# Optimization experiments

Hardware: AMD Instinct MI355X
Metric: run time of the kernel (lower is better)

The kernel has to match this reference:

```python
import jax, jax.numpy as jnp
import numpy as np

GRAY = 0.2989 + 0.5870 + 0.1140  # tf.image.rgb_to_grayscale weight sum (channels identical after grayscale_to_rgb)


def _resample(img, coords, axis):
    """Bilinear 1-D resample of `img` along `axis` at float `coords` (clamped)."""
    n = img.shape[axis]
    i0f = jnp.floor(coords)
    i0 = jnp.clip(i0f, 0, n - 1).astype(jnp.int32)
    i1 = jnp.clip(i0f + 1.0, 0, n - 1).astype(jnp.int32)
    f = coords - i0f
    a = jnp.take(img, i0, axis=axis)
    b = jnp.take(img, i1, axis=axis)
    shp = [1] * img.ndim
    shp[axis] = -1
    f = f.reshape(shp)
    return a * (1.0 - f) + b * f


def _aug_one(img, off_f, b, c, size, docrop, flp, k):
    S = img.shape[0]
    # ---- random crop (prob 0.5) + bilinear resize back to SxS (half-pixel centers) ----
    size_f = jnp.where(docrop, size.astype(jnp.float32), float(S))
    off = jnp.where(docrop, jnp.floor(off_f * (S - size_f + 1.0)), 0.0)  # [2] integer-valued offsets
    idx = (jnp.arange(S, dtype=jnp.float32) + 0.5) * (size_f / S) - 0.5
    img = _resample(img, idx + off[0], 0)
    img = _resample(img, idx + off[1], 1)
    # ---- random flip_left_right + rot90(k) ----
    img = jnp.where(flp, img[:, ::-1, :], img)
    rots = jnp.stack([img,
                      jnp.rot90(img, 1, (0, 1)),
                      jnp.rot90(img, 2, (0, 1)),
                      jnp.rot90(img, 3, (0, 1))])
    img = rots[k]
    # ---- per-channel brightness + contrast (gray->rgb->gray round trip == GRAY scale) ----
    x = img + b  # [S,S,C] + [C]
    m = jnp.mean(x, axis=(0, 1), keepdims=True)
    x = (x - m) * c + m
    return x * GRAY


def setup_inputs() -> dict:
    B, S, C = 64, 256, 5
    key = jax.random.key(0)
    ks = jax.random.split(key, 8)
    crops = jax.random.normal(ks[0], (B, S, S, C), dtype=jnp.float32)
    crop_size = jax.random.randint(ks[1], (B,), int(0.8 * S), S, dtype=jnp.int32)
    do_crop = jax.random.uniform(ks[2], (B,)) < 0.5
    off_frac = jax.random.uniform(ks[3], (B, 2), dtype=jnp.float32)
    flip = jax.random.uniform(ks[4], (B,)) < 0.5
    rot_k = jax.random.randint(ks[5], (B,), 0, 4, dtype=jnp.int32)
    bright = jax.random.uniform(ks[6], (B, C), minval=-0.1, maxval=0.1, dtype=jnp.float32)
    contrast = jax.random.uniform(ks[7], (B, C), minval=0.8, maxval=1.2, dtype=jnp.float32)
    return {"crops": crops, "off_frac": off_frac, "bright": bright, "contrast": contrast,
            "crop_size": crop_size, "do_crop": do_crop, "flip": flip, "rot_k": rot_k}


def reference(crops, off_frac, bright, contrast, crop_size, do_crop, flip, rot_k):
    return jax.vmap(_aug_one)(crops, off_frac, bright, contrast, crop_size, do_crop, flip, rot_k)
```

## Files before the change

kernel.cpp:

```cpp
#include <hip/hip_runtime.h>
#include <math.h>

#define SDIM 256
#define CH 5
#define ROWF (SDIM * CH)
#define GRAYF 0.9999f

__global__ __launch_bounds__(256) void aug_fused_kernel(
    const float* __restrict__ crops,
    const float* __restrict__ off_frac,
    const int*   __restrict__ crop_size,
    const int*   __restrict__ do_crop,
    const int*   __restrict__ flip,
    const int*   __restrict__ rot_k,
    const float* __restrict__ bright,
    const float* __restrict__ contrast,
    float* __restrict__ out)
{
    const int tid = threadIdx.x;
    const int b   = blockIdx.x & 63;
    const int pp  = blockIdx.x >> 6;

    __shared__ __align__(16) float smem[28 * 260];
    __shared__ __align__(16) float wyl[SDIM];
    __shared__ __align__(16) float wxl[SDIM];
    __shared__ float psum[4][CH];
    __shared__ float prm[2 * CH];

    const bool  docrop = do_crop[b] != 0;
    const float size_f = docrop ? (float)crop_size[b] : 256.0f;
    const float scale  = size_f * (1.0f / 256.0f);
    const float span   = 256.0f - size_f + 1.0f;
    const float off0   = docrop ? floorf(off_frac[2 * b + 0] * span) : 0.0f;
    const float off1   = docrop ? floorf(off_frac[2 * b + 1] * span) : 0.0f;
    const int   k      = rot_k[b] & 3;
    const bool  flp    = flip[b] != 0;

    wyl[tid] = 0.0f;
    wxl[tid] = 0.0f;
    __syncthreads();
    {
        const float cy = ((float)tid + 0.5f) * scale - 0.5f + off0;
        const float fl = floorf(cy);
        const float fy = cy - fl;
        const int r0 = min(max((int)fl, 0), 255);
        const int r1 = min(max((int)fl + 1, 0), 255);
        atomicAdd(&wyl[r0], 1.0f - fy);
        atomicAdd(&wyl[r1], fy);

        const float cx = ((float)tid + 0.5f) * scale - 0.5f + off1;
        const float fl2 = floorf(cx);
        const float fx  = cx - fl2;
        const int c0 = min(max((int)fl2, 0), 255);
        const int c1 = min(max((int)fl2 + 1, 0), 255);
        atomicAdd(&wxl[c0], 1.0f - fx);
        atomicAdd(&wxl[c1], fx);
    }
    __syncthreads();

    const float* srcbase = crops + (size_t)b * SDIM * ROWF;
    float acc[5] = {0.0f, 0.0f, 0.0f, 0.0f, 0.0f};
    #pragma unroll 4
    for (int it = 0; it < 64; ++it) {
        const int m = it * 256 + tid;
        const int r = m >> 6;
        const int t = m & 63;
        const float4* p4 = reinterpret_cast<const float4*>(srcbase + r * ROWF + t * 20);
        const float4 q0 = p4[0], q1 = p4[1], q2 = p4[2], q3 = p4[3], q4 = p4[4];
        const float wr = wyl[r];
        const float4 wx = reinterpret_cast<const float4*>(wxl)[t];
        const float w0 = wx.x * wr, w1 = wx.y * wr, w2 = wx.z * wr, w3 = wx.w * wr;
        acc[0] += q0.x * w0; acc[1] += q0.y * w0; acc[2] += q0.z * w0; acc[3] += q0.w * w0;
        acc[4] += q1.x * w0; acc[0] += q1.y * w1; acc[1] += q1.z * w1; acc[2] += q1.w * w1;
        acc[3] += q2.x * w1; acc[4] += q2.y * w1; acc[0] += q2.z * w2; acc[1] += q2.w * w2;
        acc[2] += q3.x * w2; acc[3] += q3.y * w2; acc[4] += q3.z * w2; acc[0] += q3.w * w3;
        acc[1] += q4.x * w3; acc[2] += q4.y * w3; acc[3] += q4.z * w3; acc[4] += q4.w * w3;
    }

    const int lane = tid & 63;
    const int wv   = tid >> 6;
    #pragma unroll
    for (int ch = 0; ch < CH; ++ch) {
        float s = acc[ch];
        #pragma unroll
        for (int o = 32; o > 0; o >>= 1) s += __shfl_down(s, o, 64);
        if (lane == 0) psum[wv][ch] = s;
    }
    __syncthreads();
    if (tid < CH) {
        const float s  = psum[0][tid] + psum[1][tid] + psum[2][tid] + psum[3][tid];
        const float m  = s * (1.0f / 65536.0f);
        const float co = contrast[b * CH + tid];
        const float br = bright[b * CH + tid];
        prm[tid]      = co * GRAYF;
        prm[CH + tid] = ((1.0f - co) * m + br) * GRAYF;
    }

    const int rr = tid >> 6;

    for (int og = 0; og < 8; ++og) {
        const int oi0 = pp * 32 + og * 4;
        __syncthreads();

        float vout[20];

        if ((k & 1) == 0) {
            const int y_min = (k == 0) ? oi0 : 255 - (oi0 + 3);
            const float cymin = ((float)y_min + 0.5f) * scale - 0.5f + off0;
            const int rbase = (int)floorf(cymin);
            const int nst   = docrop ? 5 : 4;

            const float4* src4 = reinterpret_cast<const float4*>(srcbase);
            float4* dst4 = reinterpret_cast<float4*>(smem);
            for (int i = tid; i < nst * 320; i += 256) {
                const int w  = i / 320;
                const int f4 = i - w * 320;
                const int rc = min(max(rbase + w, 0), 255);
                dst4[i] = src4[rc * 320 + f4];
            }
            __syncthreads();

            const int oi = oi0 + rr;
            const int y  = (k == 0) ? oi : 255 - oi;

            if (!docrop) {
                const float* rb = smem + (y - rbase) * ROWF;
                #pragma unroll
                for (int p = 0; p < 4; ++p) {
                    const int oj = lane + 64 * p;
                    const int xf = (k == 0) ? oj : 255 - oj;
                    const int x  = flp ? 255 - xf : xf;
                    #pragma unroll
                    for (int ch = 0; ch < CH; ++ch) vout[p * 5 + ch] = rb[x * CH + ch];
                }
            } else {
                const float cy  = ((float)y + 0.5f) * scale - 0.5f + off0;
                const float flr = floorf(cy);
                const float fy  = cy - flr;
                const float* rbA = smem + ((int)flr - rbase) * ROWF;
                const float* rbB = rbA + ROWF;
                #pragma unroll
                for (int p = 0; p < 4; ++p) {
                    const int oj = lane + 64 * p;
                    const int xf = (k == 0) ? oj : 255 - oj;
                    const int x  = flp ? 255 - xf : xf;
                    const float cx  = ((float)x + 0.5f) * scale - 0.5f + off1;
                    const float fl2 = floorf(cx);
                    const float fx  = cx - fl2;
                    const int c0 = min(max((int)fl2, 0), 255);
                    const int c1 = min(max((int)fl2 + 1, 0), 255);
                    #pragma unroll
                    for (int ch = 0; ch < CH; ++ch) {
                        const float aV = rbA[c0 * CH + ch] + fx * (rbA[c1 * CH + ch] - rbA[c0 * CH + ch]);
                        const float dV = rbB[c0 * CH + ch] + fx * (rbB[c1 * CH + ch] - rbB[c0 * CH + ch]);
                        vout[p * 5 + ch] = aV + fy * (dV - aV);
                    }
                }
            }
        } else {
            const int xfA = (k == 1) ? 255 - oi0 : oi0;
            const int xfB = (k == 1) ? 255 - (oi0 + 3) : oi0 + 3;
            const int xA = flp ? 255 - xfA : xfA;
            const int xB = flp ? 255 - xfB : xfB;
            const int xmin = min(xA, xB);

            if (!docrop) {
                const int base4 = min((xmin * CH) & ~3, ROWF - 24);
                const float4* rp = reinterpret_cast<const float4*>(
                    srcbase + (size_t)tid * ROWF + base4);
                const float4 q0 = rp[0], q1 = rp[1], q2 = rp[2];
                const float4 q3 = rp[3], q4 = rp[4], q5 = rp[5];
                smem[ 0*260+tid]=q0.x; smem[ 1*260+tid]=q0.y; smem[ 2*260+tid]=q0.z; smem[ 3*260+tid]=q0.w;
                smem[ 4*260+tid]=q1.x; smem[ 5*260+tid]=q1.y; smem[ 6*260+tid]=q1.z; smem[ 7*260+tid]=q1.w;
                smem[ 8*260+tid]=q2.x; smem[ 9*260+tid]=q2.y; smem[10*260+tid]=q2.z; smem[11*260+tid]=q2.w;
                smem[12*260+tid]=q3.x; smem[13*260+tid]=q3.y; smem[14*260+tid]=q3.z; smem[15*260+tid]=q3.w;
                smem[16*260+tid]=q4.x; smem[17*260+tid]=q4.y; smem[18*260+tid]=q4.z; smem[19*260+tid]=q4.w;
                smem[20*260+tid]=q5.x; smem[21*260+tid]=q5.y; smem[22*260+tid]=q5.z; smem[23*260+tid]=q5.w;
                __syncthreads();

                const int oi = oi0 + rr;
                const int xf = (k == 1) ? 255 - oi : oi;
                const int x  = flp ? 255 - xf : xf;
                const int slotA = x * CH - base4;
                #pragma unroll
                for (int p = 0; p < 4; ++p) {
                    const int oj = lane + 64 * p;
                    const int y  = (k == 1) ? oj : 255 - oj;
                    #pragma unroll
                    for (int ch = 0; ch < CH; ++ch)
                        vout[p * 5 + ch] = smem[(slotA + ch) * 260 + y];
                }
            } else {
                const float cxmin = ((float)xmin + 0.5f) * scale - 0.5f + off1;
                const int cbase = (int)floorf(cxmin);
                const int base4 = (cbase * CH) & ~3;
                const bool fastp = (cbase >= 0) && (cbase + 4 <= 255) && (base4 >= 0) && (base4 + 28 <= ROWF);

                if (fastp) {
                    const float4* rp = reinterpret_cast<const float4*>(
                        srcbase + (size_t)tid * ROWF + base4);
                    const float4 q0 = rp[0], q1 = rp[1], q2 = rp[2], q3 = rp[3];
                    const float4 q4 = rp[4], q5 = rp[5], q6 = rp[6];
                    smem[ 0*260+tid]=q0.x; smem[ 1*260+tid]=q0.y; smem[ 2*260+tid]=q0.z; smem[ 3*260+tid]=q0.w;
                    smem[ 4*260+tid]=q1.x; smem[ 5*260+tid]=q1.y; smem[ 6*260+tid]=q1.z; smem[ 7*260+tid]=q1.w;
                    smem[ 8*260+tid]=q2.x; smem[ 9*260+tid]=q2.y; smem[10*260+tid]=q2.z; smem[11*260+tid]=q2.w;
                    smem[12*260+tid]=q3.x; smem[13*260+tid]=q3.y; smem[14*260+tid]=q3.z; smem[15*260+tid]=q3.w;
                    smem[16*260+tid]=q4.x; smem[17*260+tid]=q4.y; smem[18*260+tid]=q4.z; smem[19*260+tid]=q4.w;
                    smem[20*260+tid]=q5.x; smem[21*260+tid]=q5.y; smem[22*260+tid]=q5.z; smem[23*260+tid]=q5.w;
                    smem[24*260+tid]=q6.x; smem[25*260+tid]=q6.y; smem[26*260+tid]=q6.z; smem[27*260+tid]=q6.w;
                } else {
                    #pragma unroll
                    for (int w = 0; w < 28; ++w) {
                        const int f2 = base4 + w + ROWF;
                        const int c2 = f2 / 5;
                        const int ch = f2 - c2 * 5;
                        const int cc = min(max(c2 - 256, 0), 255);
                        smem[w * 260 + tid] = srcbase[(size_t)tid * ROWF + cc * CH + ch];
                    }
                }
                __syncthreads();

                const int oi = oi0 + rr;
                const int xf = (k == 1) ? 255 - oi : oi;
                const int x  = flp ? 255 - xf : xf;
                const float cx  = ((float)x + 0.5f) * scale - 0.5f + off1;
                const float fl2 = floorf(cx);
                const float fx  = cx - fl2;
                const int slotA = (int)fl2 * CH - base4;
                const int slotB = slotA + CH;

                #pragma unroll
                for (int p = 0; p < 4; ++p) {
                    const int oj = lane + 64 * p;
                    const int y  = (k == 1) ? oj : 255 - oj;
                    const float cy  = ((float)y + 0.5f) * scale - 0.5f + off0;
                    const float flr = floorf(cy);
                    const float fy  = cy - flr;
                    const int r0 = min(max((int)flr, 0), 255);
                    const int r1 = min(max((int)flr + 1, 0), 255);
                    #pragma unroll
                    for (int ch = 0; ch < CH; ++ch) {
                        const float p00 = smem[(slotA + ch) * 260 + r0];
                        const float p01 = smem[(slotB + ch) * 260 + r0];
                        const float p10 = smem[(slotA + ch) * 260 + r1];
                        const float p11 = smem[(slotB + ch) * 260 + r1];
                        const float aV = p00 + fx * (p01 - p00);
                        const float dV = p10 + fx * (p11 - p10);
                        vout[p * 5 + ch] = aV + fy * (dV - aV);
                    }
                }
            }
        }

        float aa[5], ab[5];
        #pragma unroll
        for (int ch = 0; ch < CH; ++ch) { aa[ch] = prm[ch]; ab[ch] = prm[CH + ch]; }
        #pragma unroll
        for (int p = 0; p < 4; ++p)
            #pragma unroll
            for (int ch = 0; ch < CH; ++ch)
                vout[p * 5 + ch] = vout[p * 5 + ch] * aa[ch] + ab[ch];

        __syncthreads();
        #pragma unroll
        for (int p = 0; p < 4; ++p) {
            const int oj = lane + 64 * p;
            #pragma unroll
            for (int ch = 0; ch < CH; ++ch)
                smem[rr * ROWF + oj * CH + ch] = vout[p * 5 + ch];
        }
        __syncthreads();

        const float4* ob4 = reinterpret_cast<const float4*>(smem);
        float4* dst = reinterpret_cast<float4*>(out + ((size_t)b * SDIM + oi0) * ROWF);
        #pragma unroll
        for (int q = 0; q < 5; ++q) dst[q * 256 + tid] = ob4[q * 256 + tid];
    }
}

extern "C" void kernel_launch(void* const* d_in, const int* in_sizes, int n_in,
                              void* d_out, int out_size, void* d_ws, size_t ws_size,
                              hipStream_t stream) {
    const float* crops     = (const float*)d_in[0];
    const float* off_frac  = (const float*)d_in[1];
    const float* bright    = (const float*)d_in[2];
    const float* contrast  = (const float*)d_in[3];
    const int*   crop_size = (const int*)d_in[4];
    const int*   do_crop   = (const int*)d_in[5];
    const int*   flipb     = (const int*)d_in[6];
    const int*   rot_k     = (const int*)d_in[7];

    float* out = (float*)d_out;

    aug_fused_kernel<<<dim3(512), dim3(256), 0, stream>>>(
        crops, off_frac, crop_size, do_crop, flipb, rot_k, bright, contrast, out);
}
```

Before: 228.1 us.

## Split into resample kernel with partial sums plus separate affine pass

```diff
diff --git a/kernel.cpp b/kernel.cpp
--- a/kernel.cpp
+++ b/kernel.cpp
@@ -6,26 +6,25 @@
 #define ROWF (SDIM * CH)
 #define GRAYF 0.9999f
 
-__global__ __launch_bounds__(256) void aug_fused_kernel(
+__global__ __launch_bounds__(256) void aug_out_kernel(
     const float* __restrict__ crops,
     const float* __restrict__ off_frac,
     const int*   __restrict__ crop_size,
     const int*   __restrict__ do_crop,
     const int*   __restrict__ flip,
     const int*   __restrict__ rot_k,
-    const float* __restrict__ bright,
-    const float* __restrict__ contrast,
+    float* __restrict__ part,
     float* __restrict__ out)
 {
-    const int tid = threadIdx.x;
-    const int b   = blockIdx.x & 63;
-    const int pp  = blockIdx.x >> 6;
+    const int gid  = blockIdx.x;
+    const int oi0  = gid * 4;
+    const int b    = blockIdx.y;
+    const int tid  = threadIdx.x;
+    const int rr   = tid >> 6;
+    const int lane = tid & 63;
 
     __shared__ __align__(16) float smem[28 * 260];
-    __shared__ __align__(16) float wyl[SDIM];
-    __shared__ __align__(16) float wxl[SDIM];
     __shared__ float psum[4][CH];
-    __shared__ float prm[2 * CH];
 
     const bool  docrop = do_crop[b] != 0;
     const float size_f = docrop ? (float)crop_size[b] : 256.0f;
@@ -36,246 +35,233 @@
     const int   k      = rot_k[b] & 3;
     const bool  flp    = flip[b] != 0;
 
-    wyl[tid] = 0.0f;
-    wxl[tid] = 0.0f;
-    __syncthreads();
-    {
-        const float cy = ((float)tid + 0.5f) * scale - 0.5f + off0;
-        const float fl = floorf(cy);
-        const float fy = cy - fl;
-        const int r0 = min(max((int)fl, 0), 255);
-        const int r1 = min(max((int)fl + 1, 0), 255);
-        atomicAdd(&wyl[r0], 1.0f - fy);
-        atomicAdd(&wyl[r1], fy);
-
-        const float cx = ((float)tid + 0.5f) * scale - 0.5f + off1;
-        const float fl2 = floorf(cx);
-        const float fx  = cx - fl2;
-        const int c0 = min(max((int)fl2, 0), 255);
-        const int c1 = min(max((int)fl2 + 1, 0), 255);
-        atomicAdd(&wxl[c0], 1.0f - fx);
-        atomicAdd(&wxl[c1], fx);
-    }
-    __syncthreads();
-
-    const float* srcbase = crops + (size_t)b * SDIM * ROWF;
-    float acc[5] = {0.0f, 0.0f, 0.0f, 0.0f, 0.0f};
-    #pragma unroll 4
-    for (int it = 0; it < 64; ++it) {
-        const int m = it * 256 + tid;
-        const int r = m >> 6;
-        const int t = m & 63;
-        const float4* p4 = reinterpret_cast<const float4*>(srcbase + r * ROWF + t * 20);
-        const float4 q0 = p4[0], q1 = p4[1], q2 = p4[2], q3 = p4[3], q4 = p4[4];
-        const float wr = wyl[r];
-        const float4 wx = reinterpret_cast<const float4*>(wxl)[t];
-        const float w0 = wx.x * wr, w1 = wx.y * wr, w2 = wx.z * wr, w3 = wx.w * wr;
-        acc[0] += q0.x * w0; acc[1] += q0.y * w0; acc[2] += q0.z * w0; acc[3] += q0.w * w0;
-        acc[4] += q1.x * w0; acc[0] += q1.y * w1; acc[1] += q1.z * w1; acc[2] += q1.w * w1;
-        acc[3] += q2.x * w1; acc[4] += q2.y * w1; acc[0] += q2.z * w2; acc[1] += q2.w * w2;
-        acc[2] += q3.x * w2; acc[3] += q3.y * w2; acc[4] += q3.z * w2; acc[0] += q3.w * w3;
-        acc[1] += q4.x * w3; acc[2] += q4.y * w3; acc[3] += q4.z * w3; acc[4] += q4.w * w3;
-    }
-
-    const int lane = tid & 63;
-    const int wv   = tid >> 6;
-    #pragma unroll
-    for (int ch = 0; ch < CH; ++ch) {
-        float s = acc[ch];
-        #pragma unroll
-        for (int o = 32; o > 0; o >>= 1) s += __shfl_down(s, o, 64);
-        if (lane == 0) psum[wv][ch] = s;
-    }
-    __syncthreads();
-    if (tid < CH) {
-        const float s  = psum[0][tid] + psum[1][tid] + psum[2][tid] + psum[3][tid];
-        const float m  = s * (1.0f / 65536.0f);
-        const float co = contrast[b * CH + tid];
-        const float br = bright[b * CH + tid];
-        prm[tid]      = co * GRAYF;
-        prm[CH + tid] = ((1.0f - co) * m + br) * GRAYF;
-    }
-
-    const int rr = tid >> 6;
-
-    for (int og = 0; og < 8; ++og) {
-        const int oi0 = pp * 32 + og * 4;
+    float vout[20];
+
+    if ((k & 1) == 0) {
+        const int y_min = (k == 0) ? oi0 : 255 - (oi0 + 3);
+        const float cymin = ((float)y_min + 0.5f) * scale - 0.5f + off0;
+        const int rbase = (int)floorf(cymin);
+        const int nst   = docrop ? 5 : 4;
+
+        const float4* src4 = reinterpret_cast<const float4*>(crops + (size_t)b * SDIM * ROWF);
+        float4* dst4 = reinterpret_cast<float4*>(smem);
+        for (int i = tid; i < nst * 320; i += 256) {
+            const int w  = i / 320;
+            const int f4 = i - w * 320;
+            const int rc = min(max(rbase + w, 0), 255);
+            dst4[i] = src4[rc * 320 + f4];
+        }
         __syncthreads();
 
-        float vout[20];
-
-        if ((k & 1) == 0) {
-            const int y_min = (k == 0) ? oi0 : 255 - (oi0 + 3);
-            const float cymin = ((float)y_min + 0.5f) * scale - 0.5f + off0;
-            const int rbase = (int)floorf(cymin);
-            const int nst   = docrop ? 5 : 4;
-
-            const float4* src4 = reinterpret_cast<const float4*>(srcbase);
-            float4* dst4 = reinterpret_cast<float4*>(smem);
-            for (int i = tid; i < nst * 320; i += 256) {
-                const int w  = i / 320;
-                const int f4 = i - w * 320;
-                const int rc = min(max(rbase + w, 0), 255);
-                dst4[i] = src4[rc * 320 + f4];
-            }
+        const int oi = oi0 + rr;
+        const int y  = (k == 0) ? oi : 255 - oi;
+
+        if (!docrop) {
+            const float* rb = smem + (y - rbase) * ROWF;
+            #pragma unroll
+            for (int p = 0; p < 4; ++p) {
+                const int oj = lane + 64 * p;
+                const int xf = (k == 0) ? oj : 255 - oj;
+                const int x  = flp ? 255 - xf : xf;
+                #pragma unroll
+                for (int ch = 0; ch < CH; ++ch) vout[p * 5 + ch] = rb[x * CH + ch];
+            }
+        } else {
+            const float cy  = ((float)y + 0.5f) * scale - 0.5f + off0;
+            const float flr = floorf(cy);
+            const float fy  = cy - flr;
+            const float* rbA = smem + ((int)flr - rbase) * ROWF;
+            const float* rbB = rbA + ROWF;
+            #pragma unroll
+            for (int p = 0; p < 4; ++p) {
+                const int oj = lane + 64 * p;
+                const int xf = (k == 0) ? oj : 255 - oj;
+                const int x  = flp ? 255 - xf : xf;
+                const float cx  = ((float)x + 0.5f) * scale - 0.5f + off1;
+                const float fl2 = floorf(cx);
+                const float fx  = cx - fl2;
+                const int c0 = min(max((int)fl2, 0), 255);
+                const int c1 = min(max((int)fl2 + 1, 0), 255);
+                #pragma unroll
+                for (int ch = 0; ch < CH; ++ch) {
+                    const float aV = rbA[c0 * CH + ch] + fx * (rbA[c1 * CH + ch] - rbA[c0 * CH + ch]);
+                    const float dV = rbB[c0 * CH + ch] + fx * (rbB[c1 * CH + ch] - rbB[c0 * CH + ch]);
+                    vout[p * 5 + ch] = aV + fy * (dV - aV);
+                }
+            }
+        }
+    } else {
+        const int xfA = (k == 1) ? 255 - oi0 : oi0;
+        const int xfB = (k == 1) ? 255 - (oi0 + 3) : oi0 + 3;
+        const int xA = flp ? 255 - xfA : xfA;
+        const int xB = flp ? 255 - xfB : xfB;
+        const int xmin = min(xA, xB);
+
+        if (!docrop) {
+            const int base4 = min((xmin * CH) & ~3, ROWF - 24);
+            const float4* rp = reinterpret_cast<const float4*>(
+                crops + ((size_t)b * SDIM + tid) * ROWF + base4);
+            const float4 q0 = rp[0], q1 = rp[1], q2 = rp[2];
+            const float4 q3 = rp[3], q4 = rp[4], q5 = rp[5];
+            smem[ 0*260+tid]=q0.x; smem[ 1*260+tid]=q0.y; smem[ 2*260+tid]=q0.z; smem[ 3*260+tid]=q0.w;
+            smem[ 4*260+tid]=q1.x; smem[ 5*260+tid]=q1.y; smem[ 6*260+tid]=q1.z; smem[ 7*260+tid]=q1.w;
+            smem[ 8*260+tid]=q2.x; smem[ 9*260+tid]=q2.y; smem[10*260+tid]=q2.z; smem[11*260+tid]=q2.w;
+            smem[12*260+tid]=q3.x; smem[13*260+tid]=q3.y; smem[14*260+tid]=q3.z; smem[15*260+tid]=q3.w;
+            smem[16*260+tid]=q4.x; smem[17*260+tid]=q4.y; smem[18*260+tid]=q4.z; smem[19*260+tid]=q4.w;
+            smem[20*260+tid]=q5.x; smem[21*260+tid]=q5.y; smem[22*260+tid]=q5.z; smem[23*260+tid]=q5.w;
             __syncthreads();
 
             const int oi = oi0 + rr;
-            const int y  = (k == 0) ? oi : 255 - oi;
-
-            if (!docrop) {
-                const float* rb = smem + (y - rbase) * ROWF;
-                #pragma unroll
-                for (int p = 0; p < 4; ++p) {
-                    const int oj = lane + 64 * p;
-                    const int xf = (k == 0) ? oj : 255 - oj;
-                    const int x  = flp ? 255 - xf : xf;
-                    #pragma unroll
-                    for (int ch = 0; ch < CH; ++ch) vout[p * 5 + ch] = rb[x * CH + ch];
-                }
-            } else {
-                const float cy  = ((float)y + 0.5f) * scale - 0.5f + off0;
-                const float flr = floorf(cy);
-                const float fy  = cy - flr;
-                const float* rbA = smem + ((int)flr - rbase) * ROWF;
-                const float* rbB = rbA + ROWF;
-                #pragma unroll
-                for (int p = 0; p < 4; ++p) {
-                    const int oj = lane + 64 * p;
-                    const int xf = (k == 0) ? oj : 255 - oj;
-                    const int x  = flp ? 255 - xf : xf;
-                    const float cx  = ((float)x + 0.5f) * scale - 0.5f + off1;
-                    const float fl2 = floorf(cx);
-                    const float fx  = cx - fl2;
-                    const int c0 = min(max((int)fl2, 0), 255);
-                    const int c1 = min(max((int)fl2 + 1, 0), 255);
-                    #pragma unroll
-                    for (int ch = 0; ch < CH; ++ch) {
-                        const float aV = rbA[c0 * CH + ch] + fx * (rbA[c1 * CH + ch] - rbA[c0 * CH + ch]);
-                        const float dV = rbB[c0 * CH + ch] + fx * (rbB[c1 * CH + ch] - rbB[c0 * CH + ch]);
-                        vout[p * 5 + ch] = aV + fy * (dV - aV);
-                    }
-                }
+            const int xf = (k == 1) ? 255 - oi : oi;
+            const int x  = flp ? 255 - xf : xf;
+            const int slotA = x * CH - base4;
+            #pragma unroll
+            for (int p = 0; p < 4; ++p) {
+                const int oj = lane + 64 * p;
+                const int y  = (k == 1) ? oj : 255 - oj;
+                #pragma unroll
+                for (int ch = 0; ch < CH; ++ch)
+                    vout[p * 5 + ch] = smem[(slotA + ch) * 260 + y];
             }
         } else {
-            const int xfA = (k == 1) ? 255 - oi0 : oi0;
-            const int xfB = (k == 1) ? 255 - (oi0 + 3) : oi0 + 3;
-            const int xA = flp ? 255 - xfA : xfA;
-            const int xB = flp ? 255 - xfB : xfB;
-            const int xmin = min(xA, xB);
-
-            if (!docrop) {
-                const int base4 = min((xmin * CH) & ~3, ROWF - 24);
+            const float cxmin = ((float)xmin + 0.5f) * scale - 0.5f + off1;
+            const int cbase = (int)floorf(cxmin);
+            const int base4 = (cbase * CH) & ~3;
+            const bool fastp = (cbase >= 0) && (cbase + 4 <= 255) && (base4 >= 0) && (base4 + 28 <= ROWF);
+
+            if (fastp) {
                 const float4* rp = reinterpret_cast<const float4*>(
-                    srcbase + (size_t)tid * ROWF + base4);
-                const float4 q0 = rp[0], q1 = rp[1], q2 = rp[2];
-                const float4 q3 = rp[3], q4 = rp[4], q5 = rp[5];
+                    crops + ((size_t)b * SDIM + tid) * ROWF + base4);
+                const float4 q0 = rp[0], q1 = rp[1], q2 = rp[2], q3 = rp[3];
+                const float4 q4 = rp[4], q5 = rp[5], q6 = rp[6];
                 smem[ 0*260+tid]=q0.x; smem[ 1*260+tid]=q0.y; smem[ 2*260+tid]=q0.z; smem[ 3*260+tid]=q0.w;
                 smem[ 4*260+tid]=q1.x; smem[ 5*260+tid]=q1.y; smem[ 6*260+tid]=q1.z; smem[ 7*260+tid]=q1.w;
                 smem[ 8*260+tid]=q2.x; smem[ 9*260+tid]=q2.y; smem[10*260+tid]=q2.z; smem[11*260+tid]=q2.w;
                 smem[12*260+tid]=q3.x; smem[13*260+tid]=q3.y; smem[14*260+tid]=q3.z; smem[15*260+tid]=q3.w;
                 smem[16*260+tid]=q4.x; smem[17*260+tid]=q4.y; smem[18*260+tid]=q4.z; smem[19*260+tid]=q4.w;
                 smem[20*260+tid]=q5.x; smem[21*260+tid]=q5.y; smem[22*260+tid]=q5.z; smem[23*260+tid]=q5.w;
-                __syncthreads();
-
-                const int oi = oi0 + rr;
-                const int xf = (k == 1) ? 255 - oi : oi;
-                const int x  = flp ? 255 - xf : xf;
-                const int slotA = x * CH - base4;
-                #pragma unroll
-                for (int p = 0; p < 4; ++p) {
-                    const int oj = lane + 64 * p;
-                    const int y  = (k == 1) ? oj : 255 - oj;
-                    #pragma unroll
-                    for (int ch = 0; ch < CH; ++ch)
-                        vout[p * 5 + ch] = smem[(slotA + ch) * 260 + y];
+                smem[24*260+tid]=q6.x; smem[25*260+tid]=q6.y; smem[26*260+tid]=q6.z; smem[27*260+tid]=q6.w;
+            } else {
+                #pragma unroll
+                for (int w = 0; w < 28; ++w) {
+                    const int f2 = base4 + w + ROWF;
+                    const int c2 = f2 / 5;
+                    const int ch = f2 - c2 * 5;
+                    const int cc = min(max(c2 - 256, 0), 255);
+                    smem[w * 260 + tid] = crops[((size_t)b * SDIM + tid) * ROWF + cc * CH + ch];
                 }
-            } else {
-                const float cxmin = ((float)xmin + 0.5f) * scale - 0.5f + off1;
-                const int cbase = (int)floorf(cxmin);
-                const int base4 = (cbase * CH) & ~3;
-                const bool fastp = (cbase >= 0) && (cbase + 4 <= 255) && (base4 >= 0) && (base4 + 28 <= ROWF);
-
-                if (fastp) {
-                    const float4* rp = reinterpret_cast<const float4*>(
-                        srcbase + (size_t)tid * ROWF + base4);
-                    const float4 q0 = rp[0], q1 = rp[1], q2 = rp[2], q3 = rp[3];
-                    const float4 q4 = rp[4], q5 = rp[5], q6 = rp[6];
-                    smem[ 0*260+tid]=q0.x; smem[ 1*260+tid]=q0.y; smem[ 2*260+tid]=q0.z; smem[ 3*260+tid]=q0.w;
-                    smem[ 4*260+tid]=q1.x; smem[ 5*260+tid]=q1.y; smem[ 6*260+tid]=q1.z; smem[ 7*260+tid]=q1.w;
-                    smem[ 8*260+tid]=q2.x; smem[ 9*260+tid]=q2.y; smem[10*260+tid]=q2.z; smem[11*260+tid]=q2.w;
-                    smem[12*260+tid]=q3.x; smem[13*260+tid]=q3.y; smem[14*260+tid]=q3.z; smem[15*260+tid]=q3.w;
-                    smem[16*260+tid]=q4.x; smem[17*260+tid]=q4.y; smem[18*260+tid]=q4.z; smem[19*260+tid]=q4.w;
-                    smem[20*260+tid]=q5.x; smem[21*260+tid]=q5.y; smem[22*260+tid]=q5.z; smem[23*260+tid]=q5.w;
-                    smem[24*260+tid]=q6.x; smem[25*260+tid]=q6.y; smem[26*260+tid]=q6.z; smem[27*260+tid]=q6.w;
-                } else {
-                    #pragma unroll
-                    for (int w = 0; w < 28; ++w) {
-                        const int f2 = base4 + w + ROWF;
-                        const int c2 = f2 / 5;
-                        const int ch = f2 - c2 * 5;
-                        const int cc = min(max(c2 - 256, 0), 255);
-                        smem[w * 260 + tid] = srcbase[(size_t)tid * ROWF + cc * CH + ch];
-                    }
+            }
+            __syncthreads();
+
+            const int oi = oi0 + rr;
+            const int xf = (k == 1) ? 255 - oi : oi;
+            const int x  = flp ? 255 - xf : xf;
+            const float cx  = ((float)x + 0.5f) * scale - 0.5f + off1;
+            const float fl2 = floorf(cx);
+            const float fx  = cx - fl2;
+            const int slotA = (int)fl2 * CH - base4;
+            const int slotB = slotA + CH;
+
+            #pragma unroll
+            for (int p = 0; p < 4; ++p) {
+                const int oj = lane + 64 * p;
+                const int y  = (k == 1) ? oj : 255 - oj;
+                const float cy  = ((float)y + 0.5f) * scale - 0.5f + off0;
+                const float flr = floorf(cy);
+                const float fy  = cy - flr;
+                const int r0 = min(max((int)flr, 0), 255);
+                const int r1 = min(max((int)flr + 1, 0), 255);
+                #pragma unroll
+                for (int ch = 0; ch < CH; ++ch) {
+                    const float p00 = smem[(slotA + ch) * 260 + r0];
+                    const float p01 = smem[(slotB + ch) * 260 + r0];
+                    const float p10 = smem[(slotA + ch) * 260 + r1];
+                    const float p11 = smem[(slotB + ch) * 260 + r1];
+                    const float aV = p00 + fx * (p01 - p00);
+                    const float dV = p10 + fx * (p11 - p10);
+                    vout[p * 5 + ch] = aV + fy * (dV - aV);
                 }
-                __syncthreads();
-
-                const int oi = oi0 + rr;
-                const int xf = (k == 1) ? 255 - oi : oi;
-                const int x  = flp ? 255 - xf : xf;
-                const float cx  = ((float)x + 0.5f) * scale - 0.5f + off1;
-                const float fl2 = floorf(cx);
-                const float fx  = cx - fl2;
-                const int slotA = (int)fl2 * CH - base4;
-                const int slotB = slotA + CH;
-
-                #pragma unroll
-                for (int p = 0; p < 4; ++p) {
-                    const int oj = lane + 64 * p;
-                    const int y  = (k == 1) ? oj : 255 - oj;
-                    const float cy  = ((float)y + 0.5f) * scale - 0.5f + off0;
-                    const float flr = floorf(cy);
-                    const float fy  = cy - flr;
-                    const int r0 = min(max((int)flr, 0), 255);
-                    const int r1 = min(max((int)flr + 1, 0), 255);
-                    #pragma unroll
-                    for (int ch = 0; ch < CH; ++ch) {
-                        const float p00 = smem[(slotA + ch) * 260 + r0];
-                        const float p01 = smem[(slotB + ch) * 260 + r0];
-                        const float p10 = smem[(slotA + ch) * 260 + r1];
-                        const float p11 = smem[(slotB + ch) * 260 + r1];
-                        const float aV = p00 + fx * (p01 - p00);
-                        const float dV = p10 + fx * (p11 - p10);
-                        vout[p * 5 + ch] = aV + fy * (dV - aV);
-                    }
-                }
-            }
-        }
-
-        float aa[5], ab[5];
-        #pragma unroll
-        for (int ch = 0; ch < CH; ++ch) { aa[ch] = prm[ch]; ab[ch] = prm[CH + ch]; }
-        #pragma unroll
-        for (int p = 0; p < 4; ++p)
-            #pragma unroll
-            for (int ch = 0; ch < CH; ++ch)
-                vout[p * 5 + ch] = vout[p * 5 + ch] * aa[ch] + ab[ch];
-
-        __syncthreads();
-        #pragma unroll
-        for (int p = 0; p < 4; ++p) {
-            const int oj = lane + 64 * p;
-            #pragma unroll
-            for (int ch = 0; ch < CH; ++ch)
-                smem[rr * ROWF + oj * CH + ch] = vout[p * 5 + ch];
-        }
-        __syncthreads();
-
-        const float4* ob4 = reinterpret_cast<const float4*>(smem);
-        float4* dst = reinterpret_cast<float4*>(out + ((size_t)b * SDIM + oi0) * ROWF);
-        #pragma unroll
-        for (int q = 0; q < 5; ++q) dst[q * 256 + tid] = ob4[q * 256 + tid];
-    }
+            }
+        }
+    }
+
+    {
+        const int wv = tid >> 6;
+        #pragma unroll
+        for (int ch = 0; ch < CH; ++ch) {
+            float s = vout[ch] + vout[5 + ch] + vout[10 + ch] + vout[15 + ch];
+            #pragma unroll
+            for (int o = 32; o > 0; o >>= 1) s += __shfl_down(s, o, 64);
+            if (lane == 0) psum[wv][ch] = s;
+        }
+    }
+
+    __syncthreads();
+    if (tid == 0) {
+        #pragma unroll
+        for (int ch = 0; ch < CH; ++ch)
+            part[((size_t)b * 64 + gid) * CH + ch] =
+                psum[0][ch] + psum[1][ch] + psum[2][ch] + psum[3][ch];
+    }
+    #pragma unroll
+    for (int p = 0; p < 4; ++p) {
+        const int oj = lane + 64 * p;
+        #pragma unroll
+        for (int ch = 0; ch < CH; ++ch)
+            smem[rr * ROWF + oj * CH + ch] = vout[p * 5 + ch];
+    }
+    __syncthreads();
+
+    const float4* ob4 = reinterpret_cast<const float4*>(smem);
+    float4* dst = reinterpret_cast<float4*>(out + ((size_t)b * SDIM + oi0) * ROWF);
+    #pragma unroll
+    for (int q = 0; q < 5; ++q) dst[q * 256 + tid] = ob4[q * 256 + tid];
+}
+
+__global__ __launch_bounds__(256) void aug_affine_kernel(
+    const float* __restrict__ part,
+    const float* __restrict__ bright,
+    const float* __restrict__ contrast,
+    float* __restrict__ out)
+{
+    const int g   = blockIdx.x;
+    const int b   = blockIdx.y;
+    const int tid = threadIdx.x;
+
+    __shared__ float pbuf[64][CH];
+    __shared__ float prm[2 * CH];
+
+    if (tid < 64) {
+        const float* pp = part + ((size_t)b * 64 + tid) * CH;
+        #pragma unroll
+        for (int ch = 0; ch < CH; ++ch) pbuf[tid][ch] = pp[ch];
+    }
+    __syncthreads();
+    if (tid < CH) {
+        float s = 0.0f;
+        #pragma unroll
+        for (int j = 0; j < 64; ++j) s += pbuf[j][tid];
+        const float m  = s * (1.0f / 65536.0f);
+        const float co = contrast[b * CH + tid];
+        const float br = bright[b * CH + tid];
+        prm[tid]      = co * GRAYF;
+        prm[CH + tid] = ((1.0f - co) * m + br) * GRAYF;
+    }
+    __syncthreads();
+
+    float aa[5], ab[5];
+    #pragma unroll
+    for (int ch = 0; ch < CH; ++ch) { aa[ch] = prm[ch]; ab[ch] = prm[CH + ch]; }
+
+    float4* p4 = reinterpret_cast<float4*>(
+        out + ((size_t)b * SDIM + g * 4) * ROWF + tid * 20);
+    float4 q0 = p4[0], q1 = p4[1], q2 = p4[2], q3 = p4[3], q4 = p4[4];
+    q0.x = q0.x*aa[0]+ab[0]; q0.y = q0.y*aa[1]+ab[1]; q0.z = q0.z*aa[2]+ab[2]; q0.w = q0.w*aa[3]+ab[3];
+    q1.x = q1.x*aa[4]+ab[4]; q1.y = q1.y*aa[0]+ab[0]; q1.z = q1.z*aa[1]+ab[1]; q1.w = q1.w*aa[2]+ab[2];
+    q2.x = q2.x*aa[3]+ab[3]; q2.y = q2.y*aa[4]+ab[4]; q2.z = q2.z*aa[0]+ab[0]; q2.w = q2.w*aa[1]+ab[1];
+    q3.x = q3.x*aa[2]+ab[2]; q3.y = q3.y*aa[3]+ab[3]; q3.z = q3.z*aa[4]+ab[4]; q3.w = q3.w*aa[0]+ab[0];
+    q4.x = q4.x*aa[1]+ab[1]; q4.y = q4.y*aa[2]+ab[2]; q4.z = q4.z*aa[3]+ab[3]; q4.w = q4.w*aa[4]+ab[4];
+    p4[0] = q0; p4[1] = q1; p4[2] = q2; p4[3] = q3; p4[4] = q4;
 }
 
 extern "C" void kernel_launch(void* const* d_in, const int* in_sizes, int n_in,
@@ -290,8 +276,11 @@
     const int*   flipb     = (const int*)d_in[6];
     const int*   rot_k     = (const int*)d_in[7];
 
-    float* out = (float*)d_out;
-
-    aug_fused_kernel<<<dim3(512), dim3(256), 0, stream>>>(
-        crops, off_frac, crop_size, do_crop, flipb, rot_k, bright, contrast, out);
+    float* out  = (float*)d_out;
+    float* part = (float*)d_ws;
+
+    dim3 blk(256);
+    aug_out_kernel<<<dim3(64, 64), blk, 0, stream>>>(crops, off_frac, crop_size, do_crop,
+                                                     flipb, rot_k, part, out);
+    aug_affine_kernel<<<dim3(64, 64), blk, 0, stream>>>(part, bright, contrast, out);
 }
```

Result: faster. 201.5 us (-11.7%).
